# Kernel optimization log

Measured on AMD Instinct MI355X. Metric: run time of the kernel, lower is better.

Reference implementation:

```python
import jax, jax.numpy as jnp
import numpy as np

B, S, D, H, SEP = 4, 2048, 768, 8, 102
Dh = D // H


def layer_norm(x, g, b, eps=1e-5):
    m = jnp.mean(x, axis=-1, keepdims=True)
    v = jnp.var(x, axis=-1, keepdims=True)
    return (x - m) / jnp.sqrt(v + eps) * g + b


def setup_inputs() -> dict:
    key = jax.random.key(0)
    ks = jax.random.split(key, 16)
    hidden_states = jax.random.normal(ks[0], (B, S, D), dtype=jnp.float32)
    # input_ids: random vocab ids avoiding SEP, with two SEP tokens planted per row
    rng = np.random.default_rng(0)
    ids = rng.integers(103, 30000, size=(B, S))
    for b in range(B):
        ids[b, S // 3 + 7 * b] = SEP
        ids[b, 2 * S // 3 + 11 * b] = SEP
    input_ids = jnp.asarray(ids, dtype=jnp.int64)
    attention_mask = jnp.ones((B, S), dtype=jnp.int32)
    sc = 0.02
    p = {}
    p['Wq'] = jax.random.normal(ks[1], (D, D), jnp.float32) * sc
    p['bq'] = jnp.zeros((D,), jnp.float32)
    p['Wk'] = jax.random.normal(ks[2], (D, D), jnp.float32) * sc
    p['bk'] = jnp.zeros((D,), jnp.float32)
    p['Wv'] = jax.random.normal(ks[3], (D, D), jnp.float32) * sc
    p['bv'] = jnp.zeros((D,), jnp.float32)
    p['Wo'] = jax.random.normal(ks[4], (D, D), jnp.float32) * sc
    p['bo'] = jnp.zeros((D,), jnp.float32)
    p['ln1_g'] = jnp.ones((D,), jnp.float32)
    p['ln1_b'] = jnp.zeros((D,), jnp.float32)
    p['W1'] = jax.random.normal(ks[5], (D, D), jnp.float32) * sc  # d_ff = d_model
    p['b1'] = jnp.zeros((D,), jnp.float32)
    p['W2'] = jax.random.normal(ks[6], (D, D), jnp.float32) * sc
    p['b2'] = jnp.zeros((D,), jnp.float32)
    p['ln2_g'] = jnp.ones((D,), jnp.float32)
    p['ln2_b'] = jnp.zeros((D,), jnp.float32)
    p['dn_g'] = jnp.ones((D,), jnp.float32)
    p['dn_b'] = jnp.zeros((D,), jnp.float32)
    return dict(hidden_states=hidden_states, input_ids=input_ids,
                attention_mask=attention_mask, **p)


def reference(hidden_states, input_ids, attention_mask,
              Wq, bq, Wk, bk, Wv, bv, Wo, bo, ln1_g, ln1_b,
              W1, b1, W2, b2, ln2_g, ln2_b, dn_g, dn_b):
    x = hidden_states
    # --- SEP-based ragged segment discovery (vectorized over batch) ---
    sep = input_ids == SEP                       # [B,S]
    idx = jnp.arange(S)
    big = S
    first = jnp.min(jnp.where(sep, idx, big), axis=-1)                       # [B]
    second = jnp.min(jnp.where(sep & (idx[None, :] > first[:, None]), idx, big), axis=-1)
    has2 = second < big                          # >= 2 SEP tokens present
    mid = S // 2
    src_end = jnp.where(has2, first, mid)
    hyp_start = jnp.where(has2, first + 1, mid)
    hyp_end = jnp.where(has2, second, S - 1)
    src_mask = (idx[None, :] >= 1) & (idx[None, :] < src_end[:, None])       # keys [B,S]
    hyp_mask = (idx[None, :] >= hyp_start[:, None]) & (idx[None, :] < hyp_end[:, None])
    valid = jnp.any(src_mask, -1) & jnp.any(hyp_mask, -1)                    # [B]

    # --- cross-attention: queries = hyp tokens, keys/values = src tokens ---
    q = (x @ Wq + bq).reshape(B, S, H, Dh)
    k = (x @ Wk + bk).reshape(B, S, H, Dh)
    v = (x @ Wv + bv).reshape(B, S, H, Dh)
    scores = jnp.einsum('bqhd,bkhd->bhqk', q, k) / jnp.sqrt(jnp.float32(Dh))
    scores = jnp.where(src_mask[:, None, None, :], scores, jnp.float32(-1e9))
    attn = jax.nn.softmax(scores, axis=-1)
    ctx = jnp.einsum('bhqk,bkhd->bqhd', attn, v).reshape(B, S, D)
    mha = ctx @ Wo + bo
    x1 = layer_norm(x + mha, ln1_g, ln1_b)
    ffn = jax.nn.gelu(x1 @ W1 + b1) @ W2 + b2
    x2 = layer_norm(x1 + ffn, ln2_g, ln2_b)      # updated_hyp

    # --- diff + LayerNorm, scatter back into hyp segment only ---
    diff = layer_norm(x2 - x, dn_g, dn_b)
    upd = hyp_mask & valid[:, None]
    return jnp.where(upd[..., None], x + diff, x)
```

## Files before the change

### kernel.cpp

```cpp
#include <hip/hip_runtime.h>
#include <math.h>

#define BB 4
#define SS 2048
#define DD 768
#define HH 8
#define DHD 96
#define SEP_ID 102
#define CHUNK 256
#define NCH_MAX 3
#define QT64 11
#define SLOTB 12800

typedef __attribute__((ext_vector_type(8))) short bf16x8;
typedef __attribute__((ext_vector_type(4))) float f32x4;

static __device__ __forceinline__ float gelu_tanh(float x) {
  float x3 = x * x * x;
  float t = tanhf(0.7978845608028654f * (x + 0.044715f * x3));
  return 0.5f * x * (1.0f + t);
}

static __device__ __forceinline__ unsigned short f2bf(float f) {
  unsigned int u = __float_as_uint(f);
  u = (u + 0x7FFF + ((u >> 16) & 1)) >> 16;
  return (unsigned short)u;
}

static __device__ __forceinline__ float bf2f(unsigned short u) {
  return __uint_as_float(((unsigned int)u) << 16);
}

#define MFMA16(A, B, C) __builtin_amdgcn_mfma_f32_16x16x32_bf16(A, B, C, 0, 0, 0)

static __device__ __forceinline__ void gl16(const void* g, void* l) {
  __builtin_amdgcn_global_load_lds(
      (__attribute__((address_space(1))) unsigned int*)g,
      (__attribute__((address_space(3))) unsigned int*)l, 16, 0, 0);
}

__global__ __launch_bounds__(256) void prep(
    const int* __restrict__ ids, int* __restrict__ seg,
    const float* __restrict__ x, unsigned short* __restrict__ xbf, int n4,
    const float* __restrict__ W0, const float* __restrict__ W1,
    const float* __restrict__ W2, const float* __restrict__ W3,
    const float* __restrict__ W4, const float* __restrict__ W5,
    unsigned short* __restrict__ Wt) {
  __shared__ char smem[64 * 65 * 4];
  int bx = blockIdx.x;
  if (bx < 4) {
    int* s1 = (int*)smem;
    int* s2 = s1 + 256;
    int b = bx;
    const int* row = ids + (size_t)b * SS;
    int m1 = SS, m2 = SS;
    for (int i = threadIdx.x; i < SS; i += 256) {
      if (row[i] == SEP_ID) {
        if (i < m1) { m2 = m1; m1 = i; }
        else if (i < m2) { m2 = i; }
      }
    }
    s1[threadIdx.x] = m1; s2[threadIdx.x] = m2;
    __syncthreads();
    for (int off = 128; off > 0; off >>= 1) {
      if (threadIdx.x < off) {
        int a1 = s1[threadIdx.x], a2 = s2[threadIdx.x];
        int b1 = s1[threadIdx.x + off], b2 = s2[threadIdx.x + off];
        s1[threadIdx.x] = min(a1, b1);
        s2[threadIdx.x] = min(max(a1, b1), min(a2, b2));
      }
      __syncthreads();
    }
    if (threadIdx.x == 0) {
      int first = s1[0], second = s2[0];
      bool has2 = (second < SS);
      int mid = SS / 2;
      int src_end = has2 ? first : mid;
      int hyp_lo = has2 ? (first + 1) : mid;
      int hyp_hi = has2 ? second : (SS - 1);
      int valid = ((src_end - 1) > 0 && (hyp_hi - hyp_lo) > 0) ? 1 : 0;
      if (!valid) { src_end = 1; hyp_lo = 0; hyp_hi = 0; }
      seg[b * 4 + 0] = src_end;
      seg[b * 4 + 1] = hyp_lo;
      seg[b * 4 + 2] = hyp_hi;
      seg[b * 4 + 3] = valid;
    }
  } else if (bx < 1540) {
    int i = (bx - 4) * 256 + threadIdx.x;
    int stride = 1536 * 256;
    const float4* xi = (const float4*)x;
    for (; i < n4; i += stride) {
      float4 v = xi[i];
      ushort4 r;
      r.x = f2bf(v.x); r.y = f2bf(v.y); r.z = f2bf(v.z); r.w = f2bf(v.w);
      *(ushort4*)(xbf + (size_t)i * 4) = r;
    }
  } else {
    float (*t)[65] = (float(*)[65])smem;
    int idx = bx - 1540;
    int z = idx / 144, rem = idx - z * 144;
    const float* W = (z == 0) ? W0 : (z == 1) ? W1 : (z == 2) ? W2
                    : (z == 3) ? W3 : (z == 4) ? W4 : W5;
    unsigned short* O = Wt + (size_t)z * DD * DD;
    int k0 = (rem / 12) * 64, n0 = (rem % 12) * 64;
    for (int i = threadIdx.x; i < 4096; i += 256) {
      int kk = i >> 6, nn = i & 63;
      t[kk][nn] = W[(size_t)(k0 + kk) * DD + n0 + nn];
    }
    __syncthreads();
    for (int i = threadIdx.x; i < 4096; i += 256) {
      int nn = i >> 6, kk = i & 63;
      O[(size_t)(n0 + nn) * DD + k0 + kk] = f2bf(t[kk][nn]);
    }
  }
}

__device__ __forceinline__ void gemm_core(
    const unsigned short* __restrict__ A, const unsigned short* __restrict__ Wt,
    const float* __restrict__ bias, unsigned short* __restrict__ C,
    int b, int row0, int hi, int col0, int which, float rs,
    unsigned short (*Al)[64 * 64], unsigned short (*Bl)[64 * 64]) {
  int tid = threadIdx.x, w = tid >> 6, lane = tid & 63;
  int llo = lane & 15, lhi = lane >> 4;
  int wrg = w >> 1, wcg = w & 1;

  const unsigned short* Ab = A + (size_t)b * SS * DD;

  f32x4 acc[2][2];
#pragma unroll
  for (int i = 0; i < 2; ++i)
#pragma unroll
    for (int j = 0; j < 2; ++j) acc[i][j] = (f32x4){0.f, 0.f, 0.f, 0.f};

  auto STAGE = [&](int t, int buf) {
    int kk = t * 64;
#pragma unroll
    for (int j = 0; j < 2; ++j) {
      int s = j * 256 + tid;
      int row = s >> 3, c = s & 7;
      int gr = min(row0 + row, hi - 1);
      gl16(Ab + (size_t)gr * DD + kk + ((c ^ (row & 7)) * 8),
           &Al[buf][(size_t)(j * 256 + w * 64) * 8]);
    }
#pragma unroll
    for (int j = 0; j < 2; ++j) {
      int s = j * 256 + tid;
      int row = s >> 3, c = s & 7;
      gl16(Wt + (size_t)(col0 + row) * DD + kk + ((c ^ (row & 7)) * 8),
           &Bl[buf][(size_t)(j * 256 + w * 64) * 8]);
    }
  };

  STAGE(0, 0);
  __syncthreads();
  for (int t = 0; t < DD / 64; ++t) {
    int cur = t & 1;
    if (t + 1 < DD / 64) STAGE(t + 1, cur ^ 1);
#pragma unroll
    for (int ksub = 0; ksub < 2; ++ksub) {
      bf16x8 af[2], bfr[2];
#pragma unroll
      for (int mi = 0; mi < 2; ++mi) {
        int lr = wrg * 32 + mi * 16 + llo;
        int slot = lr * 8 + ((ksub * 4 + lhi) ^ (lr & 7));
        af[mi] = *(const bf16x8*)&Al[cur][(size_t)slot * 8];
      }
#pragma unroll
      for (int ni = 0; ni < 2; ++ni) {
        int lr = wcg * 32 + ni * 16 + llo;
        int slot = lr * 8 + ((ksub * 4 + lhi) ^ (lr & 7));
        bfr[ni] = *(const bf16x8*)&Bl[cur][(size_t)slot * 8];
      }
#pragma unroll
      for (int mi = 0; mi < 2; ++mi)
#pragma unroll
        for (int ni = 0; ni < 2; ++ni)
          acc[mi][ni] = MFMA16(af[mi], bfr[ni], acc[mi][ni]);
    }
    __syncthreads();
  }

  float osc = (which == 0) ? rs : 1.f;
#pragma unroll
  for (int mi = 0; mi < 2; ++mi)
#pragma unroll
    for (int ni = 0; ni < 2; ++ni) {
      int col = col0 + wcg * 32 + ni * 16 + llo;
      float bsv = bias[col];
      int rowb = row0 + wrg * 32 + mi * 16 + lhi * 4;
#pragma unroll
      for (int r = 0; r < 4; ++r) {
        int row = rowb + r;
        if (which == 2) {
          float v = acc[mi][ni][r] + bsv;
          C[((size_t)b * DD + col) * SS + row] =
              (row < hi) ? f2bf(v) : (unsigned short)0;
        } else if (row < hi) {
          float v = (acc[mi][ni][r] + bsv) * osc;
          if (which == 4) v = gelu_tanh(v);
          C[((size_t)(b * SS + row)) * DD + col] = f2bf(v);
        }
      }
    }
}

__global__ __launch_bounds__(256) void gemm_qkv(
    const unsigned short* __restrict__ A, const unsigned short* __restrict__ Wt3,
    const float* __restrict__ bq, const float* __restrict__ bk, const float* __restrict__ bv,
    unsigned short* __restrict__ Qo, unsigned short* __restrict__ Ko,
    unsigned short* __restrict__ Vto, const int* __restrict__ seg, float rs) {
  __shared__ unsigned short Al[2][64 * 64];
  __shared__ unsigned short Bl[2][64 * 64];
  int b = blockIdx.z;
  int which = blockIdx.x / 12;
  int col0 = (blockIdx.x % 12) * 64;
  int lo = (which == 0) ? seg[b * 4 + 1] : 1;
  int hi = (which == 0) ? seg[b * 4 + 2] : seg[b * 4 + 0];
  int row0 = lo + (int)blockIdx.y * 64;
  if (row0 >= hi && !(which == 2 && row0 < hi + 64)) return;
  const unsigned short* Wt = Wt3 + (size_t)which * DD * DD;
  const float* bias = (which == 0) ? bq : (which == 1) ? bk : bv;
  unsigned short* C = (which == 0) ? Qo : (which == 1) ? Ko : Vto;
  gemm_core(A, Wt, bias, C, b, row0, hi, col0, which, rs, Al, Bl);
}

__global__ __launch_bounds__(256) void gemm_mfma(
    const unsigned short* __restrict__ A, const unsigned short* __restrict__ Wt,
    const float* __restrict__ bias, unsigned short* __restrict__ C,
    const int* __restrict__ seg, int gelu) {
  __shared__ unsigned short Al[2][64 * 64];
  __shared__ unsigned short Bl[2][64 * 64];
  int b = blockIdx.z;
  int lo = seg[b * 4 + 1], hi = seg[b * 4 + 2];
  int row0 = lo + (int)blockIdx.y * 64;
  if (row0 >= hi) return;
  gemm_core(A, Wt, bias, C, b, row0, hi, (int)blockIdx.x * 64,
            gelu ? 4 : 3, 1.f, Al, Bl);
}

__global__ __launch_bounds__(256) void attn_split(
    const unsigned short* __restrict__ Q, const unsigned short* __restrict__ K,
    const unsigned short* __restrict__ Vt, char* __restrict__ part,
    const int* __restrict__ seg) {
  int bh = blockIdx.z;
  int b = bh >> 3, h = bh & 7;
  int src_hi = seg[b * 4 + 0];
  int hyp_lo = seg[b * 4 + 1], hyp_hi = seg[b * 4 + 2];
  int q0b = hyp_lo + (int)blockIdx.x * 64;
  if (q0b >= hyp_hi) return;
  int ks = 1 + (int)blockIdx.y * CHUNK;
  if (ks >= src_hi) return;
  int ke = min(ks + CHUNK, src_hi);

  __shared__ unsigned short kls[64 * 128];
  __shared__ unsigned short vls[96 * 64];
  __shared__ unsigned short plds[4][1024];

  int tid = threadIdx.x;
  int w = tid >> 6, lane = tid & 63;
  int llo = lane & 15, lhi = lane >> 4;

  int qrow = min(q0b + w * 16 + llo, hyp_hi - 1);
  const unsigned short* qbase = Q + ((size_t)(b * SS + qrow)) * DD + h * DHD;
  bf16x8 qf[3];
#pragma unroll
  for (int df = 0; df < 3; ++df)
    qf[df] = *(const bf16x8*)(qbase + df * 32 + lhi * 8);

  const unsigned short* Kb = K + (size_t)b * SS * DD + h * DHD;
  const unsigned short* Vb = Vt + ((size_t)b * DD + h * DHD) * SS;

  f32x4 acc[6];
#pragma unroll
  for (int dt = 0; dt < 6; ++dt) acc[dt] = (f32x4){0.f, 0.f, 0.f, 0.f};
  float m_r[4] = {-1e30f, -1e30f, -1e30f, -1e30f};
  float l_r[4] = {0.f, 0.f, 0.f, 0.f};

  for (int k0 = ks; k0 < ke; k0 += 64) {
    __syncthreads();
#pragma unroll
    for (int p = 0; p < 3; ++p) {
      int idx = tid + p * 256;
      int row = idx / 12, slot = idx - row * 12;
      int krow = min(k0 + row, ke - 1);
      bf16x8 v = *(const bf16x8*)(Kb + (size_t)krow * DD + slot * 8);
      *(bf16x8*)&kls[row * 128 + ((slot ^ (row & 7)) << 3)] = v;
    }
#pragma unroll
    for (int p = 0; p < 3; ++p) {
      int idx = tid + p * 256;
      int row = idx >> 3, slot = idx & 7;
      bf16x8 v = *(const bf16x8*)(Vb + (size_t)row * SS + k0 + slot * 8);
      *(bf16x8*)&vls[row * 64 + ((slot ^ (row & 7)) << 3)] = v;
    }
    __syncthreads();
    f32x4 s[4];
#pragma unroll
    for (int t = 0; t < 4; ++t) {
      f32x4 st = (f32x4){0.f, 0.f, 0.f, 0.f};
      int row = t * 16 + llo;
#pragma unroll
      for (int df = 0; df < 3; ++df) {
        int slot = df * 4 + lhi;
        bf16x8 kf = *(const bf16x8*)&kls[row * 128 + ((slot ^ (row & 7)) << 3)];
        st = MFMA16(qf[df], kf, st);
      }
      s[t] = st;
    }
    float mx[4] = {-1e30f, -1e30f, -1e30f, -1e30f};
#pragma unroll
    for (int t = 0; t < 4; ++t) {
      bool kv = (k0 + t * 16 + llo) < ke;
#pragma unroll
      for (int r = 0; r < 4; ++r) {
        float sv = kv ? s[t][r] : -1e30f;
        s[t][r] = sv;
        mx[r] = fmaxf(mx[r], sv);
      }
    }
#pragma unroll
    for (int st = 1; st < 16; st <<= 1)
#pragma unroll
      for (int r = 0; r < 4; ++r) mx[r] = fmaxf(mx[r], __shfl_xor(mx[r], st));

    float p[4][4];
#pragma unroll
    for (int r = 0; r < 4; ++r) {
      float mn = fmaxf(m_r[r], mx[r]);
      float sc = __expf(m_r[r] - mn);
      m_r[r] = mn;
      l_r[r] *= sc;
#pragma unroll
      for (int dt = 0; dt < 6; ++dt) acc[dt][r] *= sc;
      float ps = 0.f;
#pragma unroll
      for (int t = 0; t < 4; ++t) {
        float pv = (s[t][r] > -1e29f) ? __expf(s[t][r] - mn) : 0.f;
        p[t][r] = pv;
        ps += pv;
      }
#pragma unroll
      for (int st = 1; st < 16; st <<= 1) ps += __shfl_xor(ps, st);
      l_r[r] += ps;
    }
#pragma unroll
    for (int t = 0; t < 4; ++t)
#pragma unroll
      for (int r = 0; r < 4; ++r) {
        int qq = lhi * 4 + r, kk = t * 16 + llo;
        plds[w][qq * 64 + (kk ^ ((qq & 7) << 3))] = f2bf(p[t][r]);
      }
    bf16x8 pa[2];
#pragma unroll
    for (int kh = 0; kh < 2; ++kh) {
      int idx = llo * 64 + ((lhi * 8 + kh * 32) ^ ((llo & 7) << 3));
      pa[kh] = *(const bf16x8*)&plds[w][idx];
    }
#pragma unroll
    for (int dt = 0; dt < 6; ++dt) {
      int row = dt * 16 + llo;
#pragma unroll
      for (int kh = 0; kh < 2; ++kh) {
        int slot = kh * 4 + lhi;
        bf16x8 vf = *(const bf16x8*)&vls[row * 64 + ((slot ^ (row & 7)) << 3)];
        acc[dt] = MFMA16(pa[kh], vf, acc[dt]);
      }
    }
  }
  char* slot = part + (((size_t)bh * QT64 + blockIdx.x) * NCH_MAX + blockIdx.y) * SLOTB;
  unsigned short* pacc = (unsigned short*)slot;
  float* pml = (float*)(slot + 12288);
#pragma unroll
  for (int r = 0; r < 4; ++r) {
    int qq = w * 16 + lhi * 4 + r;
#pragma unroll
    for (int dt = 0; dt < 6; ++dt)
      pacc[qq * 96 + dt * 16 + llo] = f2bf(acc[dt][r]);
    if (llo == 0) { pml[qq] = m_r[r]; pml[64 + qq] = l_r[r]; }
  }
}

__global__ __launch_bounds__(128) void attn_reduce(
    const char* __restrict__ part, unsigned short* __restrict__ ctx,
    const int* __restrict__ seg) {
  int bh = blockIdx.y;
  int b = bh >> 3, h = bh & 7;
  int src_hi = seg[b * 4 + 0];
  int hyp_lo = seg[b * 4 + 1], hyp_hi = seg[b * 4 + 2];
  int q0 = hyp_lo + (int)blockIdx.x * 16;
  if (q0 >= hyp_hi) return;
  int nch = (src_hi - 1 + CHUNK - 1) / CHUNK;
  if (nch > NCH_MAX) nch = NCH_MAX;
  int sub = blockIdx.x & 3;

  __shared__ float ml[NCH_MAX][32];
  __shared__ float Mg[16], invL[16], sc[NCH_MAX][16];
  int tid = threadIdx.x;
  const char* base = part + ((size_t)bh * QT64 + (blockIdx.x >> 2)) * NCH_MAX * SLOTB;
  for (int i = tid; i < 32 * nch; i += 128) {
    int c = i >> 5, j = i & 31;
    const float* pml = (const float*)(base + c * SLOTB + 12288);
    ml[c][j] = (j < 16) ? pml[sub * 16 + j] : pml[64 + sub * 16 + (j - 16)];
  }
  __syncthreads();
  if (tid < 16) {
    float mg = -1e30f;
    for (int c = 0; c < nch; ++c) mg = fmaxf(mg, ml[c][tid]);
    float lg = 0.f;
    for (int c = 0; c < nch; ++c) lg += ml[c][16 + tid] * __expf(ml[c][tid] - mg);
    Mg[tid] = mg;
    invL[tid] = 1.f / lg;
  }
  __syncthreads();
  for (int i = tid; i < 16 * nch; i += 128) {
    int c = i >> 4, q = i & 15;
    sc[c][q] = __expf(ml[c][q] - Mg[q]);
  }
  __syncthreads();
  for (int i = tid; i < 1536; i += 128) {
    int q = i / 96, d = i - q * 96;
    float v = 0.f;
    for (int c = 0; c < nch; ++c)
      v += bf2f(((const unsigned short*)(base + c * SLOTB))[(sub * 16 + q) * 96 + d]) * sc[c][q];
    int qq = q0 + q;
    if (qq < hyp_hi)
      ctx[((size_t)(b * SS + qq)) * DD + h * DHD + d] = f2bf(v * invL[q]);
  }
}

__device__ __forceinline__ float block_sum(float v, float* sbuf) {
#pragma unroll
  for (int off = 32; off > 0; off >>= 1) v += __shfl_xor(v, off);
  int lane = threadIdx.x & 63, w = threadIdx.x >> 6;
  __syncthreads();
  if (lane == 0) sbuf[w] = v;
  __syncthreads();
  return sbuf[0] + sbuf[1] + sbuf[2] + sbuf[3];
}

__global__ __launch_bounds__(256) void ln_residual(
    const float* __restrict__ X, const unsigned short* __restrict__ Yin,
    const float* __restrict__ g, const float* __restrict__ bta,
    float* __restrict__ Out, unsigned short* __restrict__ OutBf,
    const int* __restrict__ seg) {
  int b = blockIdx.y;
  int row = seg[b * 4 + 1] + (int)blockIdx.x;
  if (row >= seg[b * 4 + 2]) return;
  __shared__ float sbuf[4];
  size_t base = ((size_t)(b * SS + row)) * DD;
  int tid = threadIdx.x;
  float v[3];
  float sum = 0.f;
#pragma unroll
  for (int r = 0; r < 3; ++r) {
    int i = tid + r * 256;
    v[r] = X[base + i] + bf2f(Yin[base + i]);
    sum += v[r];
  }
  float mean = block_sum(sum, sbuf) * (1.f / DD);
  float vs = 0.f;
#pragma unroll
  for (int r = 0; r < 3; ++r) { float d = v[r] - mean; vs += d * d; }
  float var = block_sum(vs, sbuf) * (1.f / DD);
  float inv = rsqrtf(var + 1e-5f);
#pragma unroll
  for (int r = 0; r < 3; ++r) {
    int i = tid + r * 256;
    float o = (v[r] - mean) * inv * g[i] + bta[i];
    Out[base + i] = o;
    OutBf[base + i] = f2bf(o);
  }
}

__global__ __launch_bounds__(256) void ln2_diff_scatter(
    const float* __restrict__ X, const float* __restrict__ X1,
    const unsigned short* __restrict__ T2,
    const float* __restrict__ g2, const float* __restrict__ b2,
    const float* __restrict__ gd, const float* __restrict__ bd,
    float* __restrict__ Out, const int* __restrict__ seg) {
  int b = blockIdx.y, row = blockIdx.x;
  size_t base = ((size_t)(b * SS + row)) * DD;
  int tid = threadIdx.x;
  if (row < seg[b * 4 + 1] || row >= seg[b * 4 + 2]) {
#pragma unroll
    for (int r = 0; r < 3; ++r) {
      int i = tid + r * 256;
      Out[base + i] = X[base + i];
    }
    return;
  }
  __shared__ float sbuf[4];
  float y[3], xv[3];
  float sum = 0.f;
#pragma unroll
  for (int r = 0; r < 3; ++r) {
    int i = tid + r * 256;
    y[r] = X1[base + i] + bf2f(T2[base + i]);
    xv[r] = X[base + i];
    sum += y[r];
  }
  float mean = block_sum(sum, sbuf) * (1.f / DD);
  float vs = 0.f;
#pragma unroll
  for (int r = 0; r < 3; ++r) { float d = y[r] - mean; vs += d * d; }
  float var = block_sum(vs, sbuf) * (1.f / DD);
  float inv = rsqrtf(var + 1e-5f);
  float z[3];
  float sum2 = 0.f;
#pragma unroll
  for (int r = 0; r < 3; ++r) {
    int i = tid + r * 256;
    float x2 = (y[r] - mean) * inv * g2[i] + b2[i];
    z[r] = x2 - xv[r];
    sum2 += z[r];
  }
  float mean2 = block_sum(sum2, sbuf) * (1.f / DD);
  float vs2 = 0.f;
#pragma unroll
  for (int r = 0; r < 3; ++r) { float d = z[r] - mean2; vs2 += d * d; }
  float var2 = block_sum(vs2, sbuf) * (1.f / DD);
  float inv2 = rsqrtf(var2 + 1e-5f);
#pragma unroll
  for (int r = 0; r < 3; ++r) {
    int i = tid + r * 256;
    Out[base + i] = xv[r] + (z[r] - mean2) * inv2 * gd[i] + bd[i];
  }
}

extern "C" void kernel_launch(void* const* d_in, const int* in_sizes, int n_in,
                              void* d_out, int out_size, void* d_ws, size_t ws_size,
                              hipStream_t stream) {
  const float* x = (const float*)d_in[0];
  const int* ids = (const int*)d_in[1];
  const float* Wq = (const float*)d_in[3];
  const float* bq = (const float*)d_in[4];
  const float* Wk = (const float*)d_in[5];
  const float* bk = (const float*)d_in[6];
  const float* Wv = (const float*)d_in[7];
  const float* bv = (const float*)d_in[8];
  const float* Wo = (const float*)d_in[9];
  const float* bo = (const float*)d_in[10];
  const float* ln1g = (const float*)d_in[11];
  const float* ln1b = (const float*)d_in[12];
  const float* W1 = (const float*)d_in[13];
  const float* b1 = (const float*)d_in[14];
  const float* W2 = (const float*)d_in[15];
  const float* b2 = (const float*)d_in[16];
  const float* ln2g = (const float*)d_in[17];
  const float* ln2b = (const float*)d_in[18];
  const float* dng = (const float*)d_in[19];
  const float* dnb = (const float*)d_in[20];
  float* out = (float*)d_out;

  char* ws = (char*)d_ws;
  int* seg = (int*)ws;
  size_t NBH = (size_t)BB * SS * DD * 2;
  char* Ap = ws + 256;
  char* Bp = Ap + NBH;
  char* Cp = Bp + NBH;
  char* Dp = Cp + NBH;
  char* Fp = Dp + NBH + 8192;
  char* Gp = Fp + (size_t)BB * SS * DD * 4;

  unsigned short* x_bf = (unsigned short*)Ap;
  unsigned short* ctx_bf = (unsigned short*)Ap;
  unsigned short* h1_bf = (unsigned short*)Ap;
  unsigned short* q_bf = (unsigned short*)Bp;
  unsigned short* mha_bf = (unsigned short*)Bp;
  unsigned short* k_bf = (unsigned short*)Cp;
  unsigned short* t2_bf = (unsigned short*)Cp;
  unsigned short* vt_bf = (unsigned short*)Dp;
  unsigned short* x1_bf = (unsigned short*)Dp;
  char* part = Fp;
  float* x1f = (float*)Fp;
  unsigned short* wt = (unsigned short*)Gp;
  const size_t WSZ = (size_t)DD * DD;

  const float rs = 0.1020620726159658f;

  prep<<<2404, 256, 0, stream>>>(ids, seg, x, x_bf, BB * SS * DD / 4,
                                 Wq, Wk, Wv, Wo, W1, W2, wt);

  gemm_qkv<<<dim3(36, 12, BB), 256, 0, stream>>>(
      x_bf, wt, bq, bk, bv, q_bf, k_bf, vt_bf, seg, rs);

  attn_split<<<dim3(QT64, NCH_MAX, 32), 256, 0, stream>>>(q_bf, k_bf, vt_bf, part, seg);
  attn_reduce<<<dim3(44, 32), 128, 0, stream>>>(part, ctx_bf, seg);

  gemm_mfma<<<dim3(12, 11, BB), 256, 0, stream>>>(ctx_bf, wt + 3 * WSZ, bo, mha_bf, seg, 0);
  ln_residual<<<dim3(704, BB), 256, 0, stream>>>(x, mha_bf, ln1g, ln1b, x1f, x1_bf, seg);
  gemm_mfma<<<dim3(12, 11, BB), 256, 0, stream>>>(x1_bf, wt + 4 * WSZ, b1, h1_bf, seg, 1);
  gemm_mfma<<<dim3(12, 11, BB), 256, 0, stream>>>(h1_bf, wt + 5 * WSZ, b2, t2_bf, seg, 0);
  ln2_diff_scatter<<<dim3(SS, BB), 256, 0, stream>>>(x, x1f, t2_bf, ln2g, ln2b, dng, dnb, out, seg);
}
```

Before: 154.3 us.

## Fuse K and V projections into one block sharing A tiles; enlarge attention chunk

The QKV GEMM grid drops from 36 to 24 column groups. The K and V projections now run in the same block: each staged A tile feeds two MFMA accumulator sets, for Wk and Wv, so activation loads for K/V are done once. The Q path keeps using gemm_core, whose epilogue now always scales by rs, with the non-Q callers passing 1. The attention key CHUNK also grows from 256 to 352, so fewer chunks are needed for the source segment and there are fewer partials to reduce. The trade-off is more LDS and registers per fused block, which may lower occupancy, and less parallelism in the attention split.

```diff
diff --git a/kernel.cpp b/kernel.cpp
--- a/kernel.cpp
+++ b/kernel.cpp
@@ -7,7 +7,7 @@
 #define HH 8
 #define DHD 96
 #define SEP_ID 102
-#define CHUNK 256
+#define CHUNK 352
 #define NCH_MAX 3
 #define QT64 11
 #define SLOTB 12800
@@ -180,7 +180,6 @@
     __syncthreads();
   }
 
-  float osc = (which == 0) ? rs : 1.f;
 #pragma unroll
   for (int mi = 0; mi < 2; ++mi)
 #pragma unroll
@@ -191,12 +190,8 @@
 #pragma unroll
       for (int r = 0; r < 4; ++r) {
         int row = rowb + r;
-        if (which == 2) {
-          float v = acc[mi][ni][r] + bsv;
-          C[((size_t)b * DD + col) * SS + row] =
-              (row < hi) ? f2bf(v) : (unsigned short)0;
-        } else if (row < hi) {
-          float v = (acc[mi][ni][r] + bsv) * osc;
+        if (row < hi) {
+          float v = (acc[mi][ni][r] + bsv) * rs;
           if (which == 4) v = gelu_tanh(v);
           C[((size_t)(b * SS + row)) * DD + col] = f2bf(v);
         }
@@ -210,18 +205,107 @@
     unsigned short* __restrict__ Qo, unsigned short* __restrict__ Ko,
     unsigned short* __restrict__ Vto, const int* __restrict__ seg, float rs) {
   __shared__ unsigned short Al[2][64 * 64];
-  __shared__ unsigned short Bl[2][64 * 64];
+  __shared__ unsigned short B0l[2][64 * 64];
+  __shared__ unsigned short B1l[2][64 * 64];
+  const size_t WSZ = (size_t)DD * DD;
   int b = blockIdx.z;
-  int which = blockIdx.x / 12;
   int col0 = (blockIdx.x % 12) * 64;
-  int lo = (which == 0) ? seg[b * 4 + 1] : 1;
-  int hi = (which == 0) ? seg[b * 4 + 2] : seg[b * 4 + 0];
-  int row0 = lo + (int)blockIdx.y * 64;
-  if (row0 >= hi && !(which == 2 && row0 < hi + 64)) return;
-  const unsigned short* Wt = Wt3 + (size_t)which * DD * DD;
-  const float* bias = (which == 0) ? bq : (which == 1) ? bk : bv;
-  unsigned short* C = (which == 0) ? Qo : (which == 1) ? Ko : Vto;
-  gemm_core(A, Wt, bias, C, b, row0, hi, col0, which, rs, Al, Bl);
+  int tid = threadIdx.x, w = tid >> 6, lane = tid & 63;
+  int llo = lane & 15, lhi = lane >> 4;
+  int wrg = w >> 1, wcg = w & 1;
+  const unsigned short* Ab = A + (size_t)b * SS * DD;
+
+  if (blockIdx.x < 12) {
+    int lo = seg[b * 4 + 1], hi = seg[b * 4 + 2];
+    int row0 = lo + (int)blockIdx.y * 64;
+    if (row0 >= hi) return;
+    gemm_core(A, Wt3, bq, Qo, b, row0, hi, col0, 3, rs, Al, B0l);
+    return;
+  }
+
+  int hi = seg[b * 4 + 0];
+  int row0 = 1 + (int)blockIdx.y * 64;
+  if (row0 >= hi + 64) return;
+  const unsigned short* Wk_ = Wt3 + WSZ;
+  const unsigned short* Wv_ = Wt3 + 2 * WSZ;
+
+  f32x4 accK[2][2], accV[2][2];
+#pragma unroll
+  for (int i = 0; i < 2; ++i)
+#pragma unroll
+    for (int j = 0; j < 2; ++j) {
+      accK[i][j] = (f32x4){0.f, 0.f, 0.f, 0.f};
+      accV[i][j] = (f32x4){0.f, 0.f, 0.f, 0.f};
+    }
+
+  auto STAGE = [&](int t, int buf) {
+    int kk = t * 64;
+#pragma unroll
+    for (int j = 0; j < 2; ++j) {
+      int s = j * 256 + tid;
+      int row = s >> 3, c = s & 7;
+      int gr = min(row0 + row, hi - 1);
+      gl16(Ab + (size_t)gr * DD + kk + ((c ^ (row & 7)) * 8),
+           &Al[buf][(size_t)(j * 256 + w * 64) * 8]);
+    }
+#pragma unroll
+    for (int j = 0; j < 2; ++j) {
+      int s = j * 256 + tid;
+      int row = s >> 3, c = s & 7;
+      size_t woff = (size_t)(col0 + row) * DD + kk + ((c ^ (row & 7)) * 8);
+      gl16(Wk_ + woff, &B0l[buf][(size_t)(j * 256 + w * 64) * 8]);
+      gl16(Wv_ + woff, &B1l[buf][(size_t)(j * 256 + w * 64) * 8]);
+    }
+  };
+
+  STAGE(0, 0);
+  __syncthreads();
+  for (int t = 0; t < DD / 64; ++t) {
+    int cur = t & 1;
+    if (t + 1 < DD / 64) STAGE(t + 1, cur ^ 1);
+#pragma unroll
+    for (int ksub = 0; ksub < 2; ++ksub) {
+      bf16x8 af[2], bk2[2], bv2[2];
+#pragma unroll
+      for (int mi = 0; mi < 2; ++mi) {
+        int lr = wrg * 32 + mi * 16 + llo;
+        int slot = lr * 8 + ((ksub * 4 + lhi) ^ (lr & 7));
+        af[mi] = *(const bf16x8*)&Al[cur][(size_t)slot * 8];
+      }
+#pragma unroll
+      for (int ni = 0; ni < 2; ++ni) {
+        int lr = wcg * 32 + ni * 16 + llo;
+        int slot = lr * 8 + ((ksub * 4 + lhi) ^ (lr & 7));
+        bk2[ni] = *(const bf16x8*)&B0l[cur][(size_t)slot * 8];
+        bv2[ni] = *(const bf16x8*)&B1l[cur][(size_t)slot * 8];
+      }
+#pragma unroll
+      for (int mi = 0; mi < 2; ++mi)
+#pragma unroll
+        for (int ni = 0; ni < 2; ++ni) {
+          accK[mi][ni] = MFMA16(af[mi], bk2[ni], accK[mi][ni]);
+          accV[mi][ni] = MFMA16(af[mi], bv2[ni], accV[mi][ni]);
+        }
+    }
+    __syncthreads();
+  }
+
+#pragma unroll
+  for (int mi = 0; mi < 2; ++mi)
+#pragma unroll
+    for (int ni = 0; ni < 2; ++ni) {
+      int col = col0 + wcg * 32 + ni * 16 + llo;
+      float bkv = bk[col], bvv = bv[col];
+      int rowb = row0 + wrg * 32 + mi * 16 + lhi * 4;
+#pragma unroll
+      for (int r = 0; r < 4; ++r) {
+        int row = rowb + r;
+        if (row < hi)
+          Ko[((size_t)(b * SS + row)) * DD + col] = f2bf(accK[mi][ni][r] + bkv);
+        Vto[((size_t)b * DD + col) * SS + row] =
+            (row < hi) ? f2bf(accV[mi][ni][r] + bvv) : (unsigned short)0;
+      }
+    }
 }
 
 __global__ __launch_bounds__(256) void gemm_mfma(
@@ -581,7 +665,7 @@
   prep<<<2404, 256, 0, stream>>>(ids, seg, x, x_bf, BB * SS * DD / 4,
                                  Wq, Wk, Wv, Wo, W1, W2, wt);
 
-  gemm_qkv<<<dim3(36, 12, BB), 256, 0, stream>>>(
+  gemm_qkv<<<dim3(24, 12, BB), 256, 0, stream>>>(
       x_bf, wt, bq, bk, bv, q_bf, k_bf, vt_bf, seg, rs);
 
   attn_split<<<dim3(QT64, NCH_MAX, 32), 256, 0, stream>>>(q_bf, k_bf, vt_bf, part, seg);
```

Measured after the change: 150.6 us. 2.4% less time.
